# Optimization experiments

Measured on AMD Instinct MI355X. Metric: run time of the kernel, lower is better.

The kernel has to match this reference:

```python
import jax, jax.numpy as jnp
import numpy as np

B, N, K, DEG = 128, 4096, 25, 16
BN_EPS = 1e-5


def setup_inputs() -> dict:
    key = jax.random.key(0)
    ks = jax.random.split(key, 16)

    def sp_lap(k, V):
        # fixed-degree random sparse scaled Laplacian (COO); values scaled so the
        # K=25 Chebyshev recursion x2 = 2*L@x1 - x0 stays numerically bounded
        rows = jnp.repeat(jnp.arange(V, dtype=jnp.int32), DEG)
        cols = jax.random.randint(k, (V * DEG,), 0, V, dtype=jnp.int32)
        vals = jax.random.normal(jax.random.fold_in(k, 1), (V * DEG,), jnp.float32) * 0.05
        return rows, cols, vals

    l0_rows, l0_cols, l0_vals = sp_lap(ks[0], N)
    l2_rows, l2_cols, l2_vals = sp_lap(ks[1], N // 4)
    l4_rows, l4_cols, l4_vals = sp_lap(ks[2], N // 16)

    x = jax.random.normal(ks[3], (B, N, 1), jnp.float32)
    w1 = jax.random.normal(ks[4], (1 * K, 32), jnp.float32) * 0.1
    b1 = jnp.zeros((32,), jnp.float32)
    w2 = jax.random.normal(ks[5], (32 * K, 64), jnp.float32) * 0.05
    b2 = jnp.zeros((64,), jnp.float32)
    w3 = jax.random.normal(ks[6], (64 * K, 64), jnp.float32) * 0.05
    b3 = jnp.zeros((64,), jnp.float32)
    fc1_w = jax.random.normal(ks[7], (N // 16 * 64, 512), jnp.float32) * 0.01
    fc1_b = jnp.zeros((512,), jnp.float32)
    bn_gamma = jnp.ones((512,), jnp.float32)
    bn_beta = jnp.zeros((512,), jnp.float32)
    fc2_w = jax.random.normal(ks[8], (512, 10), jnp.float32) * 0.05
    fc2_b = jnp.zeros((10,), jnp.float32)

    return dict(x=x,
                l0_rows=l0_rows, l0_cols=l0_cols, l0_vals=l0_vals,
                l2_rows=l2_rows, l2_cols=l2_cols, l2_vals=l2_vals,
                l4_rows=l4_rows, l4_cols=l4_cols, l4_vals=l4_vals,
                w1=w1, b1=b1, w2=w2, b2=b2, w3=w3, b3=b3,
                fc1_w=fc1_w, fc1_b=fc1_b, bn_gamma=bn_gamma, bn_beta=bn_beta,
                fc2_w=fc2_w, fc2_b=fc2_b)


def spmm(rows, cols, vals, xm, V):
    # sparse (V,V) @ dense (V,M) via gather + segment-sum
    return jax.ops.segment_sum(vals[:, None] * xm[cols], rows, num_segments=V)


def cheb(rows, cols, vals, x, W, b):
    # GCNCheb: Chebyshev polynomial basis T_k(L) x, k=0..K-1, then linear projection
    Bb, V, Fin = x.shape
    Kk = W.shape[0] // Fin
    x0 = jnp.transpose(x, (1, 2, 0)).reshape(V, Fin * Bb)  # (V, Fin*B)
    xs = [x0]
    x1 = spmm(rows, cols, vals, x0, V)
    xs.append(x1)
    for _ in range(2, Kk):
        x2 = 2.0 * spmm(rows, cols, vals, x1, V) - x0
        xs.append(x2)
        x0, x1 = x1, x2
    Xc = jnp.stack(xs, 0).reshape(Kk, V, Fin, Bb)          # (K, V, Fin, B)
    Xc = jnp.transpose(Xc, (3, 1, 2, 0)).reshape(Bb * V, Fin * Kk)
    return (Xc @ W + b).reshape(Bb, V, -1)


def pool4(x):
    # max-pool over consecutive groups of 4 nodes (gcn_pool_4)
    Bb, V, F = x.shape
    return x.reshape(Bb, V // 4, 4, F).max(axis=2)


def reference(x,
              l0_rows, l0_cols, l0_vals,
              l2_rows, l2_cols, l2_vals,
              l4_rows, l4_cols, l4_vals,
              w1, b1, w2, b2, w3, b3,
              fc1_w, fc1_b, bn_gamma, bn_beta, fc2_w, fc2_b):
    h = jax.nn.relu(cheb(l0_rows, l0_cols, l0_vals, x, w1, b1))
    h = pool4(h)                                             # (B, N/4, 32)
    h = jax.nn.relu(cheb(l2_rows, l2_cols, l2_vals, h, w2, b2))
    h = pool4(h)                                             # (B, N/16, 64)
    h = jax.nn.relu(cheb(l4_rows, l4_cols, l4_vals, h, w3, b3))
    h = h.reshape(h.shape[0], -1)                            # (B, N/16 * 64)
    h = h @ fc1_w + fc1_b                                    # (B, 512)
    mean = h.mean(axis=0)
    var = h.var(axis=0)  # biased, matching torch BatchNorm training normalization
    h = (h - mean) / jnp.sqrt(var + BN_EPS) * bn_gamma + bn_beta
    h = jax.nn.relu(h)
    logits = h @ fc2_w + fc2_b                               # (B, 10)
    return jax.nn.log_softmax(logits, axis=1)
```

## Files before the change

kernel.cpp:

```cpp
#include <hip/hip_runtime.h>

#define B_ 128
#define K_ 25
#define DEG_ 16

#define R4(X) X(0) X(1) X(2) X(3)

typedef __attribute__((ext_vector_type(4))) float f32x4;
typedef __attribute__((ext_vector_type(8))) short bf16x8;

__device__ __forceinline__ float4 f4ma(float t, float4 w, float4 a) {
    a.x = fmaf(t, w.x, a.x); a.y = fmaf(t, w.y, a.y);
    a.z = fmaf(t, w.z, a.z); a.w = fmaf(t, w.w, a.w);
    return a;
}
__device__ __forceinline__ float4 f4max(float4 a, float4 b) {
    return make_float4(fmaxf(a.x, b.x), fmaxf(a.y, b.y), fmaxf(a.z, b.z), fmaxf(a.w, b.w));
}
__device__ __forceinline__ float4 f4add(float4 a, float4 b) {
    return make_float4(a.x + b.x, a.y + b.y, a.z + b.z, a.w + b.w);
}
__device__ __forceinline__ float4 f4sub2(float4 s, float4 p) {
    return make_float4(2.f * s.x - p.x, 2.f * s.y - p.y, 2.f * s.z - p.z, 2.f * s.w - p.w);
}
__device__ __forceinline__ unsigned f2bfu(float f) {
    unsigned u = __float_as_uint(f);
    return (u + 0x7FFFu + ((u >> 16) & 1u)) >> 16;
}
__device__ __forceinline__ unsigned packbf(float e, float o) { return f2bfu(e) | (f2bfu(o) << 16); }
__device__ __forceinline__ float4 mevens(uint4 m) {
    return make_float4(__uint_as_float(m.x << 16), __uint_as_float(m.y << 16),
                       __uint_as_float(m.z << 16), __uint_as_float(m.w << 16));
}
__device__ __forceinline__ float4 modds(uint4 m) {
    return make_float4(__uint_as_float(m.x & 0xFFFF0000u), __uint_as_float(m.y & 0xFFFF0000u),
                       __uint_as_float(m.z & 0xFFFF0000u), __uint_as_float(m.w & 0xFFFF0000u));
}

__device__ __forceinline__ bf16x8 u2b(uint4 u) {
    union { uint4 u4; bf16x8 b8; } c; c.u4 = u; return c.b8;
}
__device__ __forceinline__ f32x4 mfma_bf(uint4 a, uint4 b, f32x4 c) {
    return __builtin_amdgcn_mfma_f32_16x16x32_bf16(u2b(a), u2b(b), c, 0, 0, 0);
}

__global__ __launch_bounds__(256) void k_transpose_x(const float* __restrict__ x, float* __restrict__ x0) {
    int i = blockIdx.x * 256 + threadIdx.x;
    int v = i >> 7, b = i & 127;
    x0[i] = x[(b << 12) + v];
}

__global__ __launch_bounds__(256) void k_packw(const float* __restrict__ w2, const float* __restrict__ w3,
        unsigned short* __restrict__ wb2, unsigned short* __restrict__ wb3) {
    int i = blockIdx.x * 256 + threadIdx.x;
    if (i < 51200) {
        int k = i >> 11, rem = i & 2047, fo = rem >> 5, fi = rem & 31;
        wb2[i] = (unsigned short)f2bfu(w2[(size_t)(fi * K_ + k) * 64 + fo]);
    }
    if (i < 102400) {
        int k = i >> 12, rem = i & 4095, fo = rem >> 6, fi = rem & 63;
        wb3[i] = (unsigned short)f2bfu(w3[(size_t)(fi * K_ + k) * 64 + fo]);
    }
}

__global__ __launch_bounds__(256) void k_spmm1(const int* __restrict__ cols, const float* __restrict__ vals,
        const float4* __restrict__ cur, const float4* __restrict__ prev,
        float4* __restrict__ next, int two) {
    int t = blockIdx.x * 256 + threadIdx.x;
    int v = t >> 5, lane = t & 31;
    int base = v * DEG_;
    float4 s0 = make_float4(0.f, 0.f, 0.f, 0.f), s1 = s0;
#pragma unroll
    for (int d = 0; d < 8; ++d) {
        s0 = f4ma(vals[base + d],     cur[((size_t)cols[base + d] << 5) + lane], s0);
        s1 = f4ma(vals[base + 8 + d], cur[((size_t)cols[base + 8 + d] << 5) + lane], s1);
    }
    float4 s = f4add(s0, s1);
    size_t idx = ((size_t)v << 5) + lane;
    if (two) {
        float4 p = prev[idx];
        s.x = 2.f * s.x - p.x; s.y = 2.f * s.y - p.y;
        s.z = 2.f * s.z - p.z; s.w = 2.f * s.w - p.w;
    }
    next[idx] = s;
}

template<int LOGF2>
__global__ __launch_bounds__(256) void k_spmm4m(const int* __restrict__ cols, const float* __restrict__ vals,
        const unsigned* __restrict__ mirPrev, float* __restrict__ st,
        unsigned* __restrict__ mirOut, int two) {
    constexpr int SL = LOGF2 + 2;
    constexpr int MSTR = 1 << (LOGF2 + 7);
    int xcd = blockIdx.x & 7, q = blockIdx.x >> 3;
    int v = __builtin_amdgcn_readfirstlane((q << (8 - SL)) + (threadIdx.x >> SL));
    int l = threadIdx.x & ((1 << SL) - 1);
    int cc = (xcd << SL) + l;
    int fi2 = cc >> 5, b0 = (cc & 31) << 2;
    int base = v * DEG_;
    int moff = (fi2 << 7) + b0;
    float4 eA = make_float4(0.f, 0.f, 0.f, 0.f), eB = eA, oA = eA, oB = eA;
#pragma unroll
    for (int d = 0; d < 8; ++d) {
        {
            float w = vals[base + d];
            uint4 m = *(const uint4*)(mirPrev + (size_t)cols[base + d] * MSTR + moff);
            eA = f4ma(w, mevens(m), eA); oA = f4ma(w, modds(m), oA);
        }
        {
            float w = vals[base + 8 + d];
            uint4 m = *(const uint4*)(mirPrev + (size_t)cols[base + 8 + d] * MSTR + moff);
            eB = f4ma(w, mevens(m), eB); oB = f4ma(w, modds(m), oB);
        }
    }
    float4 e = f4add(eA, eB), o = f4add(oA, oB);
    size_t sidx = ((size_t)v << (LOGF2 + 8)) + (fi2 << 8) + b0;
    if (two) {
        float4 pe = *(const float4*)(st + sidx), po = *(const float4*)(st + sidx + 128);
        e = f4sub2(e, pe); o = f4sub2(o, po);
    }
    *(float4*)(st + sidx) = e;
    *(float4*)(st + sidx + 128) = o;
    *(uint4*)(mirOut + (size_t)v * MSTR + moff) =
        make_uint4(packbf(e.x, o.x), packbf(e.y, o.y), packbf(e.z, o.z), packbf(e.w, o.w));
}

__global__ __launch_bounds__(256) void k_proj1_pool(const float* __restrict__ basis,
        const float* __restrict__ W1, const float* __restrict__ b1, float* __restrict__ pool1,
        unsigned* __restrict__ mir) {
    int half = blockIdx.y;
    int i = blockIdx.x * 256 + threadIdx.x;
    int g = i >> 7, b = i & 127;
    const float* wbase = W1 + half * 16;
#define P1_DM(j) float4 M##j = make_float4(-1e30f, -1e30f, -1e30f, -1e30f);
    R4(P1_DM)
#undef P1_DM
    for (int r = 0; r < 4; ++r) {
        const float* bp = basis + (((size_t)(4 * g + r) << 7) + b);
#define P1_DC(j) float4 C##j = make_float4(0.f, 0.f, 0.f, 0.f);
        R4(P1_DC)
#undef P1_DC
#pragma unroll 5
        for (int k = 0; k < K_; ++k) {
            float tv = bp[(size_t)k * 524288];
            const float4* w = (const float4*)(wbase + k * 32);
#define P1_FM(j) C##j = f4ma(tv, w[j], C##j);
            R4(P1_FM)
#undef P1_FM
        }
#define P1_MX(j) M##j = f4max(M##j, C##j);
        R4(P1_MX)
#undef P1_MX
    }
    float* op = pool1 + ((size_t)g << 12) + ((size_t)half << 11) + b;
    unsigned* mp = mir + ((size_t)g << 11) + ((size_t)half << 10) + b;
    const float* bb = b1 + half * 16;
#define P1_ST(j) { \
    float e0 = fmaxf(M##j.x + bb[4*j+0], 0.f); \
    float o0 = fmaxf(M##j.y + bb[4*j+1], 0.f); \
    float e1 = fmaxf(M##j.z + bb[4*j+2], 0.f); \
    float o1 = fmaxf(M##j.w + bb[4*j+3], 0.f); \
    op[(4*j+0)*128] = e0; op[(4*j+1)*128] = o0; \
    op[(4*j+2)*128] = e1; op[(4*j+3)*128] = o1; \
    mp[(2*j+0)*128] = packbf(e0, o0); \
    mp[(2*j+1)*128] = packbf(e1, o1); }
    R4(P1_ST)
#undef P1_ST
}

__global__ __launch_bounds__(256) void k_proj_l2m(const unsigned* __restrict__ mir, size_t slotH,
        const uint4* __restrict__ wb, float* __restrict__ acc, int k0, int init,
        const float* __restrict__ bias) {
    int wid = blockIdx.x * 4 + (threadIdx.x >> 6);
    int lane = threadIdx.x & 63;
    int lm = lane & 15, lg = lane >> 4;
    int v = wid >> 3, b0 = (wid & 7) << 4;
    float* ap = acc + ((size_t)v << 13) + b0 + (lg << 2);
    f32x4 C0, C1, C2, C3;
    if (init) {
        float q0 = bias[lm], q1 = bias[16 + lm], q2 = bias[32 + lm], q3 = bias[48 + lm];
        C0 = f32x4{q0, q0, q0, q0}; C1 = f32x4{q1, q1, q1, q1};
        C2 = f32x4{q2, q2, q2, q2}; C3 = f32x4{q3, q3, q3, q3};
    } else {
        C0 = *(const f32x4*)(ap + (size_t)lm * 128);
        C1 = *(const f32x4*)(ap + (size_t)(16 + lm) * 128);
        C2 = *(const f32x4*)(ap + (size_t)(32 + lm) * 128);
        C3 = *(const f32x4*)(ap + (size_t)(48 + lm) * 128);
    }
    const unsigned* mp0 = mir + ((size_t)v << 11) + (lg << 9) + b0 + lm;
#pragma unroll
    for (int kk = 0; kk < 5; ++kk) {
        const unsigned* mp = mp0 + (size_t)kk * slotH;
        uint4 a = make_uint4(mp[0], mp[128], mp[256], mp[384]);
        int kb = (k0 + kk) << 6;
        uint4 w0 = wb[(kb + lm) * 4 + lg];
        uint4 w1 = wb[(kb + 16 + lm) * 4 + lg];
        uint4 w2 = wb[(kb + 32 + lm) * 4 + lg];
        uint4 w3 = wb[(kb + 48 + lm) * 4 + lg];
        C0 = mfma_bf(a, w0, C0);
        C1 = mfma_bf(a, w1, C1);
        C2 = mfma_bf(a, w2, C2);
        C3 = mfma_bf(a, w3, C3);
    }
    *(f32x4*)(ap + (size_t)lm * 128) = C0;
    *(f32x4*)(ap + (size_t)(16 + lm) * 128) = C1;
    *(f32x4*)(ap + (size_t)(32 + lm) * 128) = C2;
    *(f32x4*)(ap + (size_t)(48 + lm) * 128) = C3;
}

__global__ __launch_bounds__(256) void k_proj_l3m(const unsigned* __restrict__ mir, size_t slotH,
        const uint4* __restrict__ wb, float* __restrict__ acc, int k0, int init,
        const float* __restrict__ bias, int finalrelu) {
    int wid = blockIdx.x * 4 + (threadIdx.x >> 6);
    int lane = threadIdx.x & 63;
    int lm = lane & 15, lg = lane >> 4;
    int v = wid >> 3, b0 = (wid & 7) << 4;
    float* ap = acc + ((size_t)v << 13) + b0 + (lg << 2);
    f32x4 C0, C1, C2, C3;
    if (init) {
        float q0 = bias[lm], q1 = bias[16 + lm], q2 = bias[32 + lm], q3 = bias[48 + lm];
        C0 = f32x4{q0, q0, q0, q0}; C1 = f32x4{q1, q1, q1, q1};
        C2 = f32x4{q2, q2, q2, q2}; C3 = f32x4{q3, q3, q3, q3};
    } else {
        C0 = *(const f32x4*)(ap + (size_t)lm * 128);
        C1 = *(const f32x4*)(ap + (size_t)(16 + lm) * 128);
        C2 = *(const f32x4*)(ap + (size_t)(32 + lm) * 128);
        C3 = *(const f32x4*)(ap + (size_t)(48 + lm) * 128);
    }
    const unsigned* mp0 = mir + ((size_t)v << 12) + b0 + lm;
#pragma unroll
    for (int kk = 0; kk < 5; ++kk) {
        const unsigned* mp = mp0 + (size_t)kk * slotH;
        int kb = (k0 + kk) << 6;
#pragma unroll
        for (int ks = 0; ks < 2; ++ks) {
            const unsigned* mk = mp + (size_t)((ks << 4) + (lg << 2)) * 128;
            uint4 a = make_uint4(mk[0], mk[128], mk[256], mk[384]);
            int wof = (ks << 2) + lg;
            uint4 w0 = wb[(kb + lm) * 8 + wof];
            uint4 w1 = wb[(kb + 16 + lm) * 8 + wof];
            uint4 w2 = wb[(kb + 32 + lm) * 8 + wof];
            uint4 w3 = wb[(kb + 48 + lm) * 8 + wof];
            C0 = mfma_bf(a, w0, C0);
            C1 = mfma_bf(a, w1, C1);
            C2 = mfma_bf(a, w2, C2);
            C3 = mfma_bf(a, w3, C3);
        }
    }
    if (finalrelu) {
#pragma unroll
        for (int r = 0; r < 4; ++r) {
            C0[r] = fmaxf(C0[r], 0.f); C1[r] = fmaxf(C1[r], 0.f);
            C2[r] = fmaxf(C2[r], 0.f); C3[r] = fmaxf(C3[r], 0.f);
        }
    }
    *(f32x4*)(ap + (size_t)lm * 128) = C0;
    *(f32x4*)(ap + (size_t)(16 + lm) * 128) = C1;
    *(f32x4*)(ap + (size_t)(32 + lm) * 128) = C2;
    *(f32x4*)(ap + (size_t)(48 + lm) * 128) = C3;
}

__global__ __launch_bounds__(256) void k_relu_pool_m(const float* __restrict__ acc,
        float* __restrict__ pool, unsigned* __restrict__ mir) {
    int i = blockIdx.x * 256 + threadIdx.x;
    int g = i >> 12, fi2 = (i >> 7) & 31, b = i & 127;
    const float* ap = acc + (((size_t)g << 2) << 13) + (fi2 << 8) + b;
    float me = 0.f, mo = 0.f;
#pragma unroll
    for (int r = 0; r < 4; ++r) {
        me = fmaxf(me, ap[0]); mo = fmaxf(mo, ap[128]);
        ap += 8192;
    }
    size_t po = ((size_t)g << 13) + (fi2 << 8) + b;
    pool[po] = me; pool[po + 128] = mo;
    mir[i] = packbf(me, mo);
}

__global__ __launch_bounds__(256) void k_fc1_part(const float* __restrict__ t3, const float* __restrict__ w,
                           float* __restrict__ part) {
    int blk = blockIdx.x;
    int bg = blk >> 7;
    int rs = (blk >> 1) & 63;
    int j = ((blk & 1) << 8) + threadIdx.x;
    int b0 = bg << 3;
    float a0=0.f,a1=0.f,a2=0.f,a3=0.f,a4=0.f,a5=0.f,a6=0.f,a7=0.f;
    int r0 = rs << 8;
#pragma unroll 4
    for (int row = r0; row < r0 + 256; ++row) {
        float wv = w[((size_t)row << 9) + j];
        const float4* tp = (const float4*)(t3 + ((size_t)row << 7) + b0);
        float4 t0 = tp[0], t1 = tp[1];
        a0 = fmaf(t0.x, wv, a0);
        a1 = fmaf(t0.y, wv, a1);
        a2 = fmaf(t0.z, wv, a2);
        a3 = fmaf(t0.w, wv, a3);
        a4 = fmaf(t1.x, wv, a4);
        a5 = fmaf(t1.y, wv, a5);
        a6 = fmaf(t1.z, wv, a6);
        a7 = fmaf(t1.w, wv, a7);
    }
    float* pp = part + (((size_t)(rs << 7) + b0) << 9) + j;
    pp[0*512]=a0; pp[1*512]=a1; pp[2*512]=a2; pp[3*512]=a3;
    pp[4*512]=a4; pp[5*512]=a5; pp[6*512]=a6; pp[7*512]=a7;
}

__global__ __launch_bounds__(256) void k_fc1_red(const float* __restrict__ part, const float* __restrict__ bias,
                          float* __restrict__ h) {
    int i = blockIdx.x * 256 + threadIdx.x;
    float a = bias[i & 511];
#pragma unroll 8
    for (int rs = 0; rs < 64; ++rs) a += part[((size_t)rs << 16) + i];
    h[i] = a;
}

__global__ void k_bnstats(const float* __restrict__ h, float* __restrict__ mv) {
    __shared__ float s1[128], s2[128];
    int j = blockIdx.x, t = threadIdx.x;
    float v = h[(size_t)t * 512 + j];
    s1[t] = v; s2[t] = v * v;
    __syncthreads();
    for (int o = 64; o > 0; o >>= 1) {
        if (t < o) { s1[t] += s1[t + o]; s2[t] += s2[t + o]; }
        __syncthreads();
    }
    if (t == 0) {
        float m = s1[0] * (1.f / 128.f);
        float var = s2[0] * (1.f / 128.f) - m * m;
        mv[j] = m;
        mv[512 + j] = rsqrtf(var + 1e-5f);
    }
}

__global__ void k_head(const float* __restrict__ h, const float* __restrict__ mv,
                       const float* __restrict__ gamma, const float* __restrict__ beta,
                       const float* __restrict__ w2, const float* __restrict__ b2,
                       float* __restrict__ out) {
    __shared__ float hr[512];
    __shared__ float lg[16];
    int b = blockIdx.x, t = threadIdx.x;
    for (int j = t; j < 512; j += 64) {
        float x = (h[(size_t)b * 512 + j] - mv[j]) * mv[512 + j] * gamma[j] + beta[j];
        hr[j] = fmaxf(x, 0.f);
    }
    __syncthreads();
    if (t < 10) {
        float a = b2[t];
        for (int j = 0; j < 512; ++j) a += hr[j] * w2[j * 10 + t];
        lg[t] = a;
    }
    __syncthreads();
    if (t == 0) {
        float mx = -1e30f;
        for (int q = 0; q < 10; ++q) mx = fmaxf(mx, lg[q]);
        float sum = 0.f;
        for (int q = 0; q < 10; ++q) sum += expf(lg[q] - mx);
        float ls = logf(sum) + mx;
        for (int q = 0; q < 10; ++q) out[b * 10 + q] = lg[q] - ls;
    }
}

extern "C" void kernel_launch(void* const* d_in, const int* in_sizes, int n_in,
                              void* d_out, int out_size, void* d_ws, size_t ws_size,
                              hipStream_t stream) {
    (void)in_sizes; (void)n_in; (void)out_size; (void)ws_size;
    const float* x      = (const float*)d_in[0];
    const int*   l0cols = (const int*)d_in[2];
    const float* l0vals = (const float*)d_in[3];
    const int*   l2cols = (const int*)d_in[5];
    const float* l2vals = (const float*)d_in[6];
    const int*   l4cols = (const int*)d_in[8];
    const float* l4vals = (const float*)d_in[9];
    const float* w1   = (const float*)d_in[10];
    const float* b1   = (const float*)d_in[11];
    const float* w2   = (const float*)d_in[12];
    const float* b2   = (const float*)d_in[13];
    const float* w3   = (const float*)d_in[14];
    const float* b3   = (const float*)d_in[15];
    const float* fc1w = (const float*)d_in[16];
    const float* fc1b = (const float*)d_in[17];
    const float* gam  = (const float*)d_in[18];
    const float* bet  = (const float*)d_in[19];
    const float* fc2w = (const float*)d_in[20];
    const float* fc2b = (const float*)d_in[21];
    float* out = (float*)d_out;

    const size_t S1 = 4096 * 128;
    const size_t S2 = 1024 * 4096;
    const size_t S3 = 256 * 8192;

    float* ws = (float*)d_ws;
    float* basis1 = ws;
    float* st2A   = ws + 25 * S1;
    float* st2B   = st2A + S2;
    unsigned* mir2 = (unsigned*)(st2B + S2);
    float* tailp  = (float*)(mir2 + 5 * (S2 / 2));
    float* h      = tailp;
    float* mv     = h + 65536;
    unsigned short* wb2 = (unsigned short*)(mv + 1024);
    unsigned short* wb3 = wb2 + 51200;
    float* acc2   = basis1;
    float* st3A   = st2A;
    float* st3B   = st2A + S3;
    float* acc3   = st2B;
    unsigned* mir3 = mir2;
    float* part   = basis1;

    k_packw<<<400, 256, 0, stream>>>(w2, w3, wb2, wb3);

    k_transpose_x<<<2048, 256, 0, stream>>>(x, basis1);
    for (int k = 1; k < 25; ++k) {
        const float* cur  = basis1 + (size_t)(k - 1) * S1;
        const float* prev = (k >= 2) ? basis1 + (size_t)(k - 2) * S1 : cur;
        float* next = basis1 + (size_t)k * S1;
        k_spmm1<<<512, 256, 0, stream>>>(l0cols, l0vals, (const float4*)cur,
                                         (const float4*)prev, (float4*)next, k >= 2 ? 1 : 0);
    }
    k_proj1_pool<<<dim3(512, 2), 256, 0, stream>>>(basis1, w1, b1, st2A, mir2);

    {
        float* s2[2] = {st2A, st2B};
        int cs = 0;
        for (int k = 0; k < 25; ++k) {
            if (k >= 1) {
                k_spmm4m<4><<<2048, 256, 0, stream>>>(l2cols, l2vals,
                    mir2 + (size_t)((k - 1) % 5) * (S2 / 2), s2[k & 1],
                    mir2 + (size_t)(k % 5) * (S2 / 2), k >= 2 ? 1 : 0);
            }
            if (k - cs + 1 == 5) {
                k_proj_l2m<<<2048, 256, 0, stream>>>(mir2, S2 / 2, (const uint4*)wb2, acc2, cs,
                                                     cs == 0 ? 1 : 0, b2);
                cs = k + 1;
            }
        }
    }
    k_relu_pool_m<<<4096, 256, 0, stream>>>(acc2, st3A , mir3 );

    {
        float* s3[2] = {st3A, st3B};
        int cs = 0;
        for (int k = 0; k < 25; ++k) {
            if (k >= 1) {
                k_spmm4m<5><<<1024, 256, 0, stream>>>(l4cols, l4vals,
                    mir3 + (size_t)((k - 1) % 5) * (S3 / 2), s3[k & 1],
                    mir3 + (size_t)(k % 5) * (S3 / 2), k >= 2 ? 1 : 0);
            }
            if (k - cs + 1 == 5) {
                k_proj_l3m<<<512, 256, 0, stream>>>(mir3, S3 / 2, (const uint4*)wb3, acc3, cs,
                                                    cs == 0 ? 1 : 0, b3, cs == 20 ? 1 : 0);
                cs = k + 1;
            }
        }
    }

    k_fc1_part<<<2048, 256, 0, stream>>>(acc3, fc1w, part);
    k_fc1_red<<<256, 256, 0, stream>>>(part, fc1b, h);
    k_bnstats<<<512, 128, 0, stream>>>(h, mv);
    k_head<<<128, 64, 0, stream>>>(h, mv, gam, bet, fc2w, fc2b, out);
}
```

Baseline: 808.2 us.

## Gather layer-1 Chebyshev SpMM from bf16 mirror and widen fc1 batch tile

The layer-1 Chebyshev recursion now gathers neighbour rows from a packed bf16 mirror (double-buffered) instead of fp32, which halves gather traffic. Each step still writes an fp32 basis slice for the projection and emits a fresh bf16 mirror. The transpose kernel also produces the initial mirror. Separately, fc1 partial products now cover 16 batch rows per thread instead of 8, halving grid size and weight re-reads. The risk is bf16 rounding accumulating across 24 recursion steps.

```diff
diff --git a/kernel.cpp b/kernel.cpp
--- a/kernel.cpp
+++ b/kernel.cpp
@@ -5,6 +5,7 @@
 #define DEG_ 16
 
 #define R4(X) X(0) X(1) X(2) X(3)
+#define R16(X) X(0) X(1) X(2) X(3) X(4) X(5) X(6) X(7) X(8) X(9) X(10) X(11) X(12) X(13) X(14) X(15)
 
 typedef __attribute__((ext_vector_type(4))) float f32x4;
 typedef __attribute__((ext_vector_type(8))) short bf16x8;
@@ -44,10 +45,15 @@
     return __builtin_amdgcn_mfma_f32_16x16x32_bf16(u2b(a), u2b(b), c, 0, 0, 0);
 }
 
-__global__ __launch_bounds__(256) void k_transpose_x(const float* __restrict__ x, float* __restrict__ x0) {
-    int i = blockIdx.x * 256 + threadIdx.x;
-    int v = i >> 7, b = i & 127;
-    x0[i] = x[(b << 12) + v];
+__global__ __launch_bounds__(256) void k_transpose_xm(const float* __restrict__ x,
+        float* __restrict__ x0, unsigned* __restrict__ mir) {
+    int i = blockIdx.x * 256 + threadIdx.x;
+    int v = i >> 6, bp = i & 63;
+    float e = x[((size_t)(2 * bp) << 12) + v];
+    float o = x[((size_t)(2 * bp + 1) << 12) + v];
+    x0[(v << 7) + 2 * bp] = e;
+    x0[(v << 7) + 2 * bp + 1] = o;
+    mir[(v << 6) + bp] = packbf(e, o);
 }
 
 __global__ __launch_bounds__(256) void k_packw(const float* __restrict__ w2, const float* __restrict__ w3,
@@ -63,26 +69,39 @@
     }
 }
 
-__global__ __launch_bounds__(256) void k_spmm1(const int* __restrict__ cols, const float* __restrict__ vals,
-        const float4* __restrict__ cur, const float4* __restrict__ prev,
-        float4* __restrict__ next, int two) {
-    int t = blockIdx.x * 256 + threadIdx.x;
-    int v = t >> 5, lane = t & 31;
+__global__ __launch_bounds__(256) void k_spmm1m(const int* __restrict__ cols, const float* __restrict__ vals,
+        const unsigned* __restrict__ mirPrev, const float* __restrict__ prevF,
+        float* __restrict__ nextF, unsigned* __restrict__ mirOut, int two) {
+    int i = blockIdx.x * 256 + threadIdx.x;
+    int v = i >> 4, sl = i & 15;
     int base = v * DEG_;
-    float4 s0 = make_float4(0.f, 0.f, 0.f, 0.f), s1 = s0;
+    int moff = sl << 2;
+    float4 eA = make_float4(0.f, 0.f, 0.f, 0.f), oA = eA, eB = eA, oB = eA;
 #pragma unroll
     for (int d = 0; d < 8; ++d) {
-        s0 = f4ma(vals[base + d],     cur[((size_t)cols[base + d] << 5) + lane], s0);
-        s1 = f4ma(vals[base + 8 + d], cur[((size_t)cols[base + 8 + d] << 5) + lane], s1);
-    }
-    float4 s = f4add(s0, s1);
-    size_t idx = ((size_t)v << 5) + lane;
+        {
+            float w = vals[base + d];
+            uint4 m = *(const uint4*)(mirPrev + ((size_t)cols[base + d] << 6) + moff);
+            eA = f4ma(w, mevens(m), eA); oA = f4ma(w, modds(m), oA);
+        }
+        {
+            float w = vals[base + 8 + d];
+            uint4 m = *(const uint4*)(mirPrev + ((size_t)cols[base + 8 + d] << 6) + moff);
+            eB = f4ma(w, mevens(m), eB); oB = f4ma(w, modds(m), oB);
+        }
+    }
+    float4 e = f4add(eA, eB), o = f4add(oA, oB);
+    float4 f0 = make_float4(e.x, o.x, e.y, o.y);
+    float4 f1 = make_float4(e.z, o.z, e.w, o.w);
+    size_t sidx = ((size_t)v << 7) + (sl << 3);
     if (two) {
-        float4 p = prev[idx];
-        s.x = 2.f * s.x - p.x; s.y = 2.f * s.y - p.y;
-        s.z = 2.f * s.z - p.z; s.w = 2.f * s.w - p.w;
-    }
-    next[idx] = s;
+        float4 p0 = *(const float4*)(prevF + sidx), p1 = *(const float4*)(prevF + sidx + 4);
+        f0 = f4sub2(f0, p0); f1 = f4sub2(f1, p1);
+    }
+    *(float4*)(nextF + sidx) = f0;
+    *(float4*)(nextF + sidx + 4) = f1;
+    *(uint4*)(mirOut + ((size_t)v << 6) + moff) =
+        make_uint4(packbf(f0.x, f0.y), packbf(f0.z, f0.w), packbf(f1.x, f1.y), packbf(f1.z, f1.w));
 }
 
 template<int LOGF2>
@@ -278,29 +297,32 @@
 __global__ __launch_bounds__(256) void k_fc1_part(const float* __restrict__ t3, const float* __restrict__ w,
                            float* __restrict__ part) {
     int blk = blockIdx.x;
-    int bg = blk >> 7;
+    int bg4 = blk >> 7;
     int rs = (blk >> 1) & 63;
     int j = ((blk & 1) << 8) + threadIdx.x;
-    int b0 = bg << 3;
-    float a0=0.f,a1=0.f,a2=0.f,a3=0.f,a4=0.f,a5=0.f,a6=0.f,a7=0.f;
+    int b0 = bg4 << 4;
+#define FC_DA(q) float a##q = 0.f;
+    R16(FC_DA)
+#undef FC_DA
     int r0 = rs << 8;
 #pragma unroll 4
     for (int row = r0; row < r0 + 256; ++row) {
         float wv = w[((size_t)row << 9) + j];
         const float4* tp = (const float4*)(t3 + ((size_t)row << 7) + b0);
-        float4 t0 = tp[0], t1 = tp[1];
-        a0 = fmaf(t0.x, wv, a0);
-        a1 = fmaf(t0.y, wv, a1);
-        a2 = fmaf(t0.z, wv, a2);
-        a3 = fmaf(t0.w, wv, a3);
-        a4 = fmaf(t1.x, wv, a4);
-        a5 = fmaf(t1.y, wv, a5);
-        a6 = fmaf(t1.z, wv, a6);
-        a7 = fmaf(t1.w, wv, a7);
+        float4 t0 = tp[0], t1 = tp[1], t2 = tp[2], t3v = tp[3];
+        a0 = fmaf(t0.x, wv, a0);   a1 = fmaf(t0.y, wv, a1);
+        a2 = fmaf(t0.z, wv, a2);   a3 = fmaf(t0.w, wv, a3);
+        a4 = fmaf(t1.x, wv, a4);   a5 = fmaf(t1.y, wv, a5);
+        a6 = fmaf(t1.z, wv, a6);   a7 = fmaf(t1.w, wv, a7);
+        a8 = fmaf(t2.x, wv, a8);   a9 = fmaf(t2.y, wv, a9);
+        a10 = fmaf(t2.z, wv, a10); a11 = fmaf(t2.w, wv, a11);
+        a12 = fmaf(t3v.x, wv, a12); a13 = fmaf(t3v.y, wv, a13);
+        a14 = fmaf(t3v.z, wv, a14); a15 = fmaf(t3v.w, wv, a15);
     }
     float* pp = part + (((size_t)(rs << 7) + b0) << 9) + j;
-    pp[0*512]=a0; pp[1*512]=a1; pp[2*512]=a2; pp[3*512]=a3;
-    pp[4*512]=a4; pp[5*512]=a5; pp[6*512]=a6; pp[7*512]=a7;
+#define FC_ST(q) pp[q * 512] = a##q;
+    R16(FC_ST)
+#undef FC_ST
 }
 
 __global__ __launch_bounds__(256) void k_fc1_red(const float* __restrict__ part, const float* __restrict__ bias,
@@ -397,6 +419,7 @@
     float* mv     = h + 65536;
     unsigned short* wb2 = (unsigned short*)(mv + 1024);
     unsigned short* wb3 = wb2 + 51200;
+    unsigned* mir1 = (unsigned*)(wb3 + 102400);
     float* acc2   = basis1;
     float* st3A   = st2A;
     float* st3B   = st2A + S3;
@@ -406,13 +429,13 @@
 
     k_packw<<<400, 256, 0, stream>>>(w2, w3, wb2, wb3);
 
-    k_transpose_x<<<2048, 256, 0, stream>>>(x, basis1);
+    k_transpose_xm<<<1024, 256, 0, stream>>>(x, basis1, mir1 );
     for (int k = 1; k < 25; ++k) {
-        const float* cur  = basis1 + (size_t)(k - 1) * S1;
-        const float* prev = (k >= 2) ? basis1 + (size_t)(k - 2) * S1 : cur;
-        float* next = basis1 + (size_t)k * S1;
-        k_spmm1<<<512, 256, 0, stream>>>(l0cols, l0vals, (const float4*)cur,
-                                         (const float4*)prev, (float4*)next, k >= 2 ? 1 : 0);
+        const float* prevF = (k >= 2) ? basis1 + (size_t)(k - 2) * S1 : basis1;
+        float* nextF = basis1 + (size_t)k * S1;
+        k_spmm1m<<<256, 256, 0, stream>>>(l0cols, l0vals,
+            mir1 + (size_t)((k - 1) & 1) * (S1 / 2), prevF, nextF,
+            mir1 + (size_t)(k & 1) * (S1 / 2), k >= 2 ? 1 : 0);
     }
     k_proj1_pool<<<dim3(512, 2), 256, 0, stream>>>(basis1, w1, b1, st2A, mir2);
 
@@ -451,7 +474,7 @@
         }
     }
 
-    k_fc1_part<<<2048, 256, 0, stream>>>(acc3, fc1w, part);
+    k_fc1_part<<<1024, 256, 0, stream>>>(acc3, fc1w, part);
     k_fc1_red<<<256, 256, 0, stream>>>(part, fc1b, h);
     k_bnstats<<<512, 128, 0, stream>>>(h, mv);
     k_head<<<128, 64, 0, stream>>>(h, mv, gam, bet, fc2w, fc2b, out);
```

New measurement: 807.0 us. About the same (-0.2%).
